# Optimization experiments

Measured on AMD Instinct MI355X. Metric: run time of the kernel, lower is better.

## Reference

```python
import jax, jax.numpy as jnp
import numpy as np

B, N, DIM, H, DH = 4, 4096, 1024, 16, 64
INNER = H * DH


def setup_inputs() -> dict:
    key = jax.random.key(0)
    k1, k2, k3, k4 = jax.random.split(key, 4)
    x = jax.random.normal(k1, (B, N, DIM), dtype=jnp.float32)
    mask = jax.random.randint(k2, (B, N), 0, 2).astype(bool)
    Wqkv = jax.random.normal(k3, (DIM, 3 * INNER), dtype=jnp.float32) * (DIM ** -0.5)
    Wout = jax.random.normal(k4, (INNER, DIM), dtype=jnp.float32) * (INNER ** -0.5)
    bout = jnp.zeros((DIM,), dtype=jnp.float32)
    return {"x": x, "mask": mask, "Wqkv": Wqkv, "Wout": Wout, "bout": bout}


def _split_heads(t):
    b, n, _ = t.shape
    return t.reshape(b, n, H, DH).transpose(0, 2, 1, 3)  # b h n d


def reference(x, mask, Wqkv, Wout, bout):
    qkv = x @ Wqkv                      # [b, n, 3*inner]
    q, k, v = jnp.split(qkv, 3, axis=-1)
    q, k, v = map(_split_heads, (q, k, v))  # [b, h, n, d]
    q = jax.nn.elu(q) + 1.0
    k = jax.nn.elu(k) + 1.0
    m = mask[:, None, :, None]          # [b, 1, n, 1]
    k = jnp.where(m, k, 0.0)
    v = jnp.where(m, v, 0.0)
    kv = jnp.einsum('bhnd,bhne->bhde', k, v)      # [b, h, d, d]
    out = jnp.einsum('bhnd,bhde->bhne', q, kv)    # [b, h, n, d]
    z = 1.0 / (jnp.einsum('bhnd,bhd->bhn', q, k.sum(axis=2)) + 1e-6)
    out = out * z[..., None]
    out = out.transpose(0, 2, 1, 3).reshape(x.shape[0], -1, INNER)  # [b, n, inner]
    return out @ Wout + bout
```

## Files before the change

### kernel.cpp

```cpp
#include <hip/hip_runtime.h>
#include <hip/hip_bf16.h>
#include <cstddef>
#include <cstdint>

#define B_     4
#define N_     4096
#define DIM_   1024
#define H_     16
#define DH_    64
#define INNER_ 1024
#define MTOK   (B_ * N_)
#define QKVC   (3 * INNER_)
#define NCH    16
#define CHUNK  (N_ / NCH)

typedef __attribute__((ext_vector_type(8))) short short8;
typedef __attribute__((ext_vector_type(4))) float f32x4;

__device__ __forceinline__ float elu1(float x) {
    return x > 0.f ? x + 1.f : __expf(x);
}
__device__ __forceinline__ unsigned short f2bf(float f) {
    __hip_bfloat16 h = __float2bfloat16(f);
    return __builtin_bit_cast(unsigned short, h);
}
__device__ __forceinline__ float bf2f(unsigned short u) {
    __hip_bfloat16 h = __builtin_bit_cast(__hip_bfloat16, u);
    return __bfloat162float(h);
}

__device__ __forceinline__ void gload16(const void* g, void* l) {
    __builtin_amdgcn_global_load_lds(
        (const __attribute__((address_space(1))) unsigned int*)g,
        (__attribute__((address_space(3))) unsigned int*)l, 16, 0, 0);
}

__global__ __launch_bounds__(256) void cast_bf16(
    const float* __restrict__ src, unsigned short* __restrict__ dst, long n8)
{
    const long stride = (long)gridDim.x * 256;
    for (long i = (long)blockIdx.x * 256 + threadIdx.x; i < n8; i += stride) {
        const float4 f0 = reinterpret_cast<const float4*>(src)[2 * i];
        const float4 f1 = reinterpret_cast<const float4*>(src)[2 * i + 1];
        short8 u;
        u[0] = (short)f2bf(f0.x); u[1] = (short)f2bf(f0.y);
        u[2] = (short)f2bf(f0.z); u[3] = (short)f2bf(f0.w);
        u[4] = (short)f2bf(f1.x); u[5] = (short)f2bf(f1.y);
        u[6] = (short)f2bf(f1.z); u[7] = (short)f2bf(f1.w);
        reinterpret_cast<short8*>(dst)[i] = u;
    }
}

__global__ __launch_bounds__(256) void transpose_cast(
    const float* __restrict__ src, unsigned short* __restrict__ dst,
    int R, int C)
{
    __shared__ float t[32][33];
    const int r0 = blockIdx.x * 32, c0 = blockIdx.y * 32;
    const int tx = threadIdx.x & 31, ty = threadIdx.x >> 5;
#pragma unroll
    for (int i = 0; i < 4; ++i)
        t[ty * 4 + i][tx] = src[(size_t)(r0 + ty * 4 + i) * C + c0 + tx];
    __syncthreads();
#pragma unroll
    for (int i = 0; i < 4; ++i)
        dst[(size_t)(c0 + ty * 4 + i) * R + r0 + tx] = f2bf(t[tx][ty * 4 + i]);
}

template<int EPI, int HAS_BIAS>
__global__ __launch_bounds__(512, 2) void gemm256(
    const unsigned short* __restrict__ A,
    const unsigned short* __restrict__ BT,
    void* __restrict__ Cv,
    const float* __restrict__ bias,
    const int* __restrict__ msk,
    int M, int N, int K, int lda, int ldb, int ldc)
{
    __shared__ __align__(16) unsigned short smem[4][256 * 64];

    const int tid = threadIdx.x;
    const int wv  = tid >> 6;
    const int ln  = tid & 63;
    const int wr  = wv >> 2;
    const int wc  = wv & 3;

    const int nwg = gridDim.x;
    int wg = blockIdx.x;
    {
        const int q = nwg >> 3, r = nwg & 7;
        const int xcd = wg & 7, lid = wg >> 3;
        wg = (xcd < r ? xcd * (q + 1) : r * (q + 1) + (xcd - r) * q) + lid;
    }
    const int ncol = N >> 8;
    const int bx = wg % ncol;
    const int by = wg / ncol;
    const int row0 = by << 8;
    const int col0 = bx << 8;

    const int l8    = ln >> 3;
    const int sslot = ((ln & 7) ^ l8) << 3;

    const int lr16 = ln & 15;
    const int kc   = ln >> 4;
    const int sw   = lr16 & 7;
    const int soff0 = (kc ^ sw) << 3;
    const int soff1 = ((4 + kc) ^ sw) << 3;

    f32x4 acc[8][4];
#pragma unroll
    for (int m = 0; m < 8; ++m)
#pragma unroll
        for (int n = 0; n < 4; ++n) acc[m][n] = f32x4{0.f, 0.f, 0.f, 0.f};

    const int NT = K >> 6;

#pragma unroll
    for (int i = 0; i < 4; ++i) {
        const int lr = wv * 32 + i * 8;
        gload16(&A [(size_t)(row0 + lr + l8) * lda + sslot], &smem[0][lr * 64]);
        gload16(&BT[(size_t)(col0 + lr + l8) * ldb + sslot], &smem[2][lr * 64]);
    }
    __syncthreads();

    for (int t = 0; t < NT; ++t) {
        const int cur = t & 1;
        const unsigned short* bufA = smem[cur];
        const unsigned short* bufB = smem[2 + cur];
        short8 bf[4][2];
#pragma unroll
        for (int p = 0; p < 4; ++p) {
            short8 af[2][2];
#pragma unroll
            for (int mi = 0; mi < 2; ++mi) {
                const int row = wr * 128 + (p * 2 + mi) * 16 + lr16;
                af[mi][0] = *reinterpret_cast<const short8*>(&bufA[row * 64 + soff0]);
                af[mi][1] = *reinterpret_cast<const short8*>(&bufA[row * 64 + soff1]);
            }
            if (p == 0) {
#pragma unroll
                for (int n = 0; n < 4; ++n) {
                    const int row = wc * 64 + n * 16 + lr16;
                    bf[n][0] = *reinterpret_cast<const short8*>(&bufB[row * 64 + soff0]);
                    bf[n][1] = *reinterpret_cast<const short8*>(&bufB[row * 64 + soff1]);
                }
                if (t + 1 < NT) {
                    const int k0 = (t + 1) << 6;
                    unsigned short* nA = smem[cur ^ 1];
                    unsigned short* nB = smem[2 + (cur ^ 1)];
#pragma unroll
                    for (int i = 0; i < 4; ++i) {
                        const int lr = wv * 32 + i * 8;
                        gload16(&A [(size_t)(row0 + lr + l8) * lda + k0 + sslot],
                                &nA[lr * 64]);
                        gload16(&BT[(size_t)(col0 + lr + l8) * ldb + k0 + sslot],
                                &nB[lr * 64]);
                    }
                }
            }
            __builtin_amdgcn_s_barrier();
            __builtin_amdgcn_sched_barrier(0);
            __builtin_amdgcn_s_setprio(1);
#pragma unroll
            for (int mi = 0; mi < 2; ++mi)
#pragma unroll
                for (int n = 0; n < 4; ++n) {
                    acc[p * 2 + mi][n] = __builtin_amdgcn_mfma_f32_16x16x32_bf16(
                        af[mi][0], bf[n][0], acc[p * 2 + mi][n], 0, 0, 0);
                    acc[p * 2 + mi][n] = __builtin_amdgcn_mfma_f32_16x16x32_bf16(
                        af[mi][1], bf[n][1], acc[p * 2 + mi][n], 0, 0, 0);
                }
            __builtin_amdgcn_s_setprio(0);
            __builtin_amdgcn_sched_barrier(0);
            if (p < 3) {
                __builtin_amdgcn_s_barrier();
                __builtin_amdgcn_sched_barrier(0);
            }
        }
        __syncthreads();
    }

    const int orow = (ln >> 4) << 2;
    const int ocol = ln & 15;

    if constexpr (EPI == 2) {
        unsigned short* tb = &smem[0][0];
#pragma unroll
        for (int m = 0; m < 8; ++m) {
            const int rrb = wr * 128 + m * 16 + orow;
            const int4 m4 = *reinterpret_cast<const int4*>(&msk[row0 + rrb]);
            int mv[4] = { m4.x, m4.y, m4.z, m4.w };
            const int slot16 = rrb >> 3, half = (rrb >> 2) & 1;
#pragma unroll
            for (int n = 0; n < 4; ++n) {
                const int chl = wc * 64 + n * 16 + ocol;
                const bool isk = (col0 + chl) < 1024;
                ushort4 st;
#pragma unroll
                for (int r2 = 0; r2 < 4; ++r2) {
                    float o = acc[m][n][r2];
                    o = mv[r2] ? (isk ? elu1(o) : o) : 0.f;
                    ((unsigned short*)&st)[r2] = f2bf(o);
                }
                *reinterpret_cast<ushort4*>(
                    &tb[chl * 256 + ((slot16 ^ (chl & 7)) << 3) + half * 4]) = st;
            }
        }
        __syncthreads();
        unsigned short* dst = (unsigned short*)Cv;
#pragma unroll
        for (int i = 0; i < 16; ++i) {
            const int idx = i * 512 + tid;
            const int ch = idx >> 5;
            const int sl = idx & 31;
            const short8 v = *reinterpret_cast<const short8*>(
                &tb[ch * 256 + ((sl ^ (ch & 7)) << 3)]);
            *reinterpret_cast<short8*>(
                &dst[(size_t)(col0 + ch) * ldc + row0 + sl * 8]) = v;
        }
    } else {
#pragma unroll
        for (int m = 0; m < 8; ++m) {
            const int rrb = row0 + wr * 128 + m * 16 + orow;
#pragma unroll
            for (int n = 0; n < 4; ++n) {
                const int c = col0 + wc * 64 + n * 16 + ocol;
                float bv = 0.f;
                if constexpr (HAS_BIAS) bv = bias[c];
#pragma unroll
                for (int r2 = 0; r2 < 4; ++r2) {
                    const int rr = rrb + r2;
                    float o = acc[m][n][r2] + bv;
                    if constexpr (EPI == 1) {
                        o = elu1(o);
                        ((unsigned short*)Cv)[(size_t)rr * ldc + c] = f2bf(o);
                    } else {
                        ((float*)Cv)[(size_t)rr * ldc + c] = o;
                    }
                }
            }
        }
    }
}

__global__ __launch_bounds__(256) void kv_partial(
    const unsigned short* __restrict__ kvT, float* __restrict__ part)
{
    const int bh = blockIdx.x;
    const int ch = blockIdx.y;
    const int b = bh / H_, h = bh % H_;
    const int tok0 = b * N_ + ch * CHUNK;

    __shared__ __align__(16) unsigned short kt[64 * 64];
    __shared__ __align__(16) unsigned short vt[64 * 64];
    __shared__ float ksr[4][64];

    const int tid = threadIdx.x;
    const int wv = tid >> 6, ln = tid & 63;
    const int wr = wv >> 1, wc = wv & 1;
    const int l8 = ln >> 3;
    const int sslot = ((ln & 7) ^ l8) << 3;
    const int lr16 = ln & 15;
    const int kc = ln >> 4;
    const int sw = lr16 & 7;

    const size_t krow = (size_t)(h * 64) * MTOK;
    const size_t vrow = (size_t)(1024 + h * 64) * MTOK;

    f32x4 acc[2][2];
#pragma unroll
    for (int i = 0; i < 2; ++i)
#pragma unroll
        for (int j = 0; j < 2; ++j) acc[i][j] = f32x4{0.f, 0.f, 0.f, 0.f};

    const int kd = tid & 63, kq = tid >> 6;
    float ksacc = 0.f;

    for (int st = 0; st < 4; ++st) {
        const int tb = tok0 + st * 64;
        __syncthreads();
#pragma unroll
        for (int i = 0; i < 2; ++i) {
            const int rb = (wv * 2 + i) * 8;
            gload16(&kvT[krow + (size_t)(rb + l8) * MTOK + tb + sslot], &kt[rb * 64]);
            gload16(&kvT[vrow + (size_t)(rb + l8) * MTOK + tb + sslot], &vt[rb * 64]);
        }
        __syncthreads();
#pragma unroll
        for (int ks = 0; ks < 2; ++ks) {
            const int soff = ((ks * 4 + kc) ^ sw) << 3;
            short8 af[2], bf[2];
#pragma unroll
            for (int mi = 0; mi < 2; ++mi)
                af[mi] = *reinterpret_cast<const short8*>(
                    &kt[(wr * 32 + mi * 16 + lr16) * 64 + soff]);
#pragma unroll
            for (int ni = 0; ni < 2; ++ni)
                bf[ni] = *reinterpret_cast<const short8*>(
                    &vt[(wc * 32 + ni * 16 + lr16) * 64 + soff]);
#pragma unroll
            for (int mi = 0; mi < 2; ++mi)
#pragma unroll
                for (int ni = 0; ni < 2; ++ni)
                    acc[mi][ni] = __builtin_amdgcn_mfma_f32_16x16x32_bf16(
                        af[mi], bf[ni], acc[mi][ni], 0, 0, 0);
        }
#pragma unroll
        for (int sl = 0; sl < 2; ++sl) {
            const int phys = (kq * 2 + sl) ^ (kd & 7);
            short8 v = *reinterpret_cast<const short8*>(&kt[kd * 64 + phys * 8]);
#pragma unroll
            for (int e = 0; e < 8; ++e) ksacc += bf2f((unsigned short)v[e]);
        }
    }
    ksr[kq][kd] = ksacc;
    __syncthreads();

    float* p = part + ((size_t)bh * NCH + ch) * 4160;
    const int orow = (ln >> 4) << 2;
    const int ocol = ln & 15;
#pragma unroll
    for (int mi = 0; mi < 2; ++mi)
#pragma unroll
        for (int ni = 0; ni < 2; ++ni) {
            const int d0 = wr * 32 + mi * 16 + orow;
            const int e  = wc * 32 + ni * 16 + ocol;
#pragma unroll
            for (int r = 0; r < 4; ++r)
                p[(d0 + r) * 64 + e] = acc[mi][ni][r];
        }
    if (tid < 64)
        p[4096 + tid] = ksr[0][tid] + ksr[1][tid] + ksr[2][tid] + ksr[3][tid];
}

__global__ __launch_bounds__(256) void kv_reduce(
    const float* __restrict__ part, unsigned short* __restrict__ kvtb,
    float* __restrict__ ksumf)
{
    const int bh = blockIdx.x;
    for (int idx = threadIdx.x; idx < 4096; idx += 256) {
        float s = 0.f;
        for (int c = 0; c < NCH; ++c)
            s += part[((size_t)bh * NCH + c) * 4160 + idx];
        const int d = idx >> 6, e = idx & 63;
        const unsigned short hi = f2bf(s);
        const float lo = s - bf2f(hi);
        kvtb[(size_t)bh * 8192 + e * 64 + d] = hi;
        kvtb[(size_t)bh * 8192 + 4096 + e * 64 + d] = f2bf(lo);
    }
    if (threadIdx.x < 64) {
        float s = 0.f;
        for (int c = 0; c < NCH; ++c)
            s += part[((size_t)bh * NCH + c) * 4160 + 4096 + threadIdx.x];
        ksumf[bh * 64 + threadIdx.x] = s;
    }
}

__global__ __launch_bounds__(256) void attn_mfma(
    const unsigned short* __restrict__ qbf,
    const unsigned short* __restrict__ kvtb,
    const float* __restrict__ ksumf,
    unsigned short* __restrict__ attnbf)
{
    const int bh = blockIdx.x, tt = blockIdx.y;
    const int b = bh / H_, h = bh % H_;
    const int tok0 = b * N_ + tt * 256;

    __shared__ __align__(16) unsigned short qt[256 * 64];
    __shared__ float den[256];

    const int tid = threadIdx.x;
    const int wv = tid >> 6, ln = tid & 63;
    const int l8 = ln >> 3;
    const int sslot = ((ln & 7) ^ l8) << 3;
    const int lr16 = ln & 15;
    const int kc = ln >> 4;

    const unsigned short* kvb = kvtb + (size_t)bh * 8192;
    short8 bhf[4][2], blf[4][2];
#pragma unroll
    for (int n = 0; n < 4; ++n)
#pragma unroll
        for (int ks = 0; ks < 2; ++ks) {
            const int off = (n * 16 + lr16) * 64 + ks * 32 + kc * 8;
            bhf[n][ks] = *reinterpret_cast<const short8*>(&kvb[off]);
            blf[n][ks] = *reinterpret_cast<const short8*>(&kvb[4096 + off]);
        }

#pragma unroll
    for (int i = 0; i < 8; ++i) {
        const int rb = wv * 64 + i * 8;
        gload16(&qbf[(size_t)(tok0 + rb + l8) * INNER_ + h * 64 + sslot],
                &qt[rb * 64]);
    }

    {
        float dsum = 0.f;
        const unsigned short* qr = &qbf[(size_t)(tok0 + tid) * INNER_ + h * 64];
        const float* ksp = &ksumf[bh * 64];
#pragma unroll
        for (int j = 0; j < 8; ++j) {
            short8 v = *reinterpret_cast<const short8*>(&qr[j * 8]);
#pragma unroll
            for (int e = 0; e < 8; ++e)
                dsum += bf2f((unsigned short)v[e]) * ksp[j * 8 + e];
        }
        den[tid] = dsum;
    }
    __syncthreads();

    f32x4 acc[4][4];
#pragma unroll
    for (int m = 0; m < 4; ++m)
#pragma unroll
        for (int n = 0; n < 4; ++n) acc[m][n] = f32x4{0.f, 0.f, 0.f, 0.f};

#pragma unroll
    for (int ks = 0; ks < 2; ++ks) {
        const int soff = ((ks * 4 + kc) ^ (lr16 & 7)) << 3;
        short8 af[4];
#pragma unroll
        for (int m = 0; m < 4; ++m)
            af[m] = *reinterpret_cast<const short8*>(
                &qt[(wv * 64 + m * 16 + lr16) * 64 + soff]);
#pragma unroll
        for (int m = 0; m < 4; ++m)
#pragma unroll
            for (int n = 0; n < 4; ++n) {
                acc[m][n] = __builtin_amdgcn_mfma_f32_16x16x32_bf16(
                    af[m], bhf[n][ks], acc[m][n], 0, 0, 0);
                acc[m][n] = __builtin_amdgcn_mfma_f32_16x16x32_bf16(
                    af[m], blf[n][ks], acc[m][n], 0, 0, 0);
            }
    }

    const int orow = (ln >> 4) << 2;
    const int ocol = ln & 15;
#pragma unroll
    for (int m = 0; m < 4; ++m) {
        const int rl = wv * 64 + m * 16 + orow;
#pragma unroll
        for (int r = 0; r < 4; ++r) {
            const float z = 1.f / (den[rl + r] + 1e-6f);
            const size_t orow_g = (size_t)(tok0 + rl + r) * INNER_ + h * 64;
#pragma unroll
            for (int n = 0; n < 4; ++n)
                attnbf[orow_g + n * 16 + ocol] = f2bf(acc[m][n][r] * z);
        }
    }
}

extern "C" void kernel_launch(void* const* d_in, const int* in_sizes, int n_in,
                              void* d_out, int out_size, void* d_ws, size_t ws_size,
                              hipStream_t stream)
{
    const float* x    = (const float*)d_in[0];
    const int*   mask = (const int*)d_in[1];
    const float* Wqkv = (const float*)d_in[2];
    const float* Wout = (const float*)d_in[3];
    const float* bout = (const float*)d_in[4];
    float* out = (float*)d_out;

    const size_t need = 127156224;
    if (ws_size < need) return;

    char* base = (char*)d_ws;
    unsigned short* xbf    = (unsigned short*)base;
    unsigned short* attnbf = xbf;
    unsigned short* kvT    = (unsigned short*)(base + 33554432);
    unsigned short* wqkvT  = (unsigned short*)(base + 100663296);
    unsigned short* woutT  = (unsigned short*)(base + 106954752);
    float* part  = (float*)(base + 109051904);
    unsigned short* kvtb = (unsigned short*)(base + 126091264);
    float* ksumf = (float*)(base + 127139840);
    unsigned short* qbf = (unsigned short*)d_out;

    cast_bf16<<<dim3(2048), dim3(256), 0, stream>>>(
        x, xbf, (long)MTOK * DIM_ / 8);
    transpose_cast<<<dim3(32, 96), dim3(256), 0, stream>>>(Wqkv, wqkvT, DIM_, QKVC);
    transpose_cast<<<dim3(32, 32), dim3(256), 0, stream>>>(Wout, woutT, INNER_, INNER_);

    gemm256<1, 0><<<dim3(64 * 4), dim3(512), 0, stream>>>(
        xbf, wqkvT, qbf, nullptr, nullptr, MTOK, 1024, DIM_, DIM_, DIM_, 1024);
    gemm256<2, 0><<<dim3(64 * 8), dim3(512), 0, stream>>>(
        xbf, wqkvT + (size_t)1024 * 1024, kvT, nullptr, mask,
        MTOK, 2048, DIM_, DIM_, DIM_, MTOK);

    kv_partial<<<dim3(B_ * H_, NCH), dim3(256), 0, stream>>>(kvT, part);
    kv_reduce<<<dim3(B_ * H_), dim3(256), 0, stream>>>(part, kvtb, ksumf);

    attn_mfma<<<dim3(B_ * H_, N_ / 256), dim3(256), 0, stream>>>(
        qbf, kvtb, ksumf, attnbf);

    gemm256<0, 1><<<dim3(64 * 4), dim3(512), 0, stream>>>(
        attnbf, woutT, out, bout, nullptr, MTOK, INNER_, INNER_, INNER_, INNER_, INNER_);
}
```

Before: 244.0 us.

## Fuse QKV GEMMs into one launch and split K-tiles into halves with vmcnt pipelining

Merges the separate Q and KV projection GEMMs into a single 768-block launch whose epilogue branches on column block: it writes elu+1 Q row-major, or masked and transposed K/V into the kvT buffer. The GEMM main loop now stores each 64-wide K tile as two 32-wide halves with a new XOR swizzle. It prefetches per half and uses partial vmcnt waits instead of full syncthreads, aiming to overlap global loads with MFMA and cut barrier stalls. The risk is that finer-grained waits and a new swizzle could add LDS bank conflicts or sync errors, and the fused grid has mixed epilogue costs.

Result: slower. 258.7 us (+6.0%).

```diff
diff --git a/kernel.cpp b/kernel.cpp
--- a/kernel.cpp
+++ b/kernel.cpp
@@ -72,11 +72,12 @@
     const unsigned short* __restrict__ A,
     const unsigned short* __restrict__ BT,
     void* __restrict__ Cv,
+    unsigned short* __restrict__ Ckv,
     const float* __restrict__ bias,
     const int* __restrict__ msk,
     int M, int N, int K, int lda, int ldb, int ldc)
 {
-    __shared__ __align__(16) unsigned short smem[4][256 * 64];
+    __shared__ __align__(16) unsigned short smem[4][2][256 * 32];
 
     const int tid = threadIdx.x;
     const int wv  = tid >> 6;
@@ -97,14 +98,12 @@
     const int row0 = by << 8;
     const int col0 = bx << 8;
 
-    const int l8    = ln >> 3;
-    const int sslot = ((ln & 7) ^ l8) << 3;
+    const int lrow  = ln >> 2;
+    const int gslot = (((ln & 3) ^ ((ln >> 2) & 3) ^ ((ln >> 4) & 3)) << 3);
 
     const int lr16 = ln & 15;
     const int kc   = ln >> 4;
-    const int sw   = lr16 & 7;
-    const int soff0 = (kc ^ sw) << 3;
-    const int soff1 = ((4 + kc) ^ sw) << 3;
+    const int physoff = ((kc ^ ((lr16 ^ (lr16 >> 2)) & 3)) << 3);
 
     f32x4 acc[8][4];
 #pragma unroll
@@ -115,107 +114,118 @@
     const int NT = K >> 6;
 
 #pragma unroll
-    for (int i = 0; i < 4; ++i) {
-        const int lr = wv * 32 + i * 8;
-        gload16(&A [(size_t)(row0 + lr + l8) * lda + sslot], &smem[0][lr * 64]);
-        gload16(&BT[(size_t)(col0 + lr + l8) * ldb + sslot], &smem[2][lr * 64]);
-    }
-    __syncthreads();
+    for (int kh = 0; kh < 2; ++kh)
+#pragma unroll
+        for (int i = 0; i < 2; ++i) {
+            const int rowb = wv * 32 + i * 16;
+            gload16(&A [(size_t)(row0 + rowb + lrow) * lda + kh * 32 + gslot],
+                    &smem[0][kh][rowb * 32]);
+            gload16(&BT[(size_t)(col0 + rowb + lrow) * ldb + kh * 32 + gslot],
+                    &smem[2][kh][rowb * 32]);
+        }
+    asm volatile("s_waitcnt vmcnt(4)" ::: "memory");
+    __builtin_amdgcn_s_barrier();
+    __builtin_amdgcn_sched_barrier(0);
 
     for (int t = 0; t < NT; ++t) {
-        const int cur = t & 1;
-        const unsigned short* bufA = smem[cur];
-        const unsigned short* bufB = smem[2 + cur];
-        short8 bf[4][2];
-#pragma unroll
-        for (int p = 0; p < 4; ++p) {
-            short8 af[2][2];
-#pragma unroll
-            for (int mi = 0; mi < 2; ++mi) {
-                const int row = wr * 128 + (p * 2 + mi) * 16 + lr16;
-                af[mi][0] = *reinterpret_cast<const short8*>(&bufA[row * 64 + soff0]);
-                af[mi][1] = *reinterpret_cast<const short8*>(&bufA[row * 64 + soff1]);
-            }
-            if (p == 0) {
-#pragma unroll
-                for (int n = 0; n < 4; ++n) {
-                    const int row = wc * 64 + n * 16 + lr16;
-                    bf[n][0] = *reinterpret_cast<const short8*>(&bufB[row * 64 + soff0]);
-                    bf[n][1] = *reinterpret_cast<const short8*>(&bufB[row * 64 + soff1]);
+        const int buf = t & 1;
+#pragma unroll
+        for (int kh = 0; kh < 2; ++kh) {
+            const unsigned short* pA = &smem[buf][kh][0];
+            const unsigned short* pB = &smem[2 + buf][kh][0];
+            short8 af[8], bfr[4];
+#pragma unroll
+            for (int m = 0; m < 8; ++m)
+                af[m] = *reinterpret_cast<const short8*>(
+                    &pA[(wr * 128 + m * 16 + lr16) * 32 + physoff]);
+#pragma unroll
+            for (int n = 0; n < 4; ++n)
+                bfr[n] = *reinterpret_cast<const short8*>(
+                    &pB[(wc * 64 + n * 16 + lr16) * 32 + physoff]);
+            if (t + 1 < NT) {
+                const int k0 = (t + 1) * 64 + kh * 32;
+                unsigned short* nA = &smem[buf ^ 1][kh][0];
+                unsigned short* nB = &smem[2 + (buf ^ 1)][kh][0];
+#pragma unroll
+                for (int i = 0; i < 2; ++i) {
+                    const int rowb = wv * 32 + i * 16;
+                    gload16(&A [(size_t)(row0 + rowb + lrow) * lda + k0 + gslot],
+                            &nA[rowb * 32]);
+                    gload16(&BT[(size_t)(col0 + rowb + lrow) * ldb + k0 + gslot],
+                            &nB[rowb * 32]);
                 }
-                if (t + 1 < NT) {
-                    const int k0 = (t + 1) << 6;
-                    unsigned short* nA = smem[cur ^ 1];
-                    unsigned short* nB = smem[2 + (cur ^ 1)];
-#pragma unroll
-                    for (int i = 0; i < 4; ++i) {
-                        const int lr = wv * 32 + i * 8;
-                        gload16(&A [(size_t)(row0 + lr + l8) * lda + k0 + sslot],
-                                &nA[lr * 64]);
-                        gload16(&BT[(size_t)(col0 + lr + l8) * ldb + k0 + sslot],
-                                &nB[lr * 64]);
-                    }
-                }
-            }
+            }
+            __builtin_amdgcn_sched_barrier(0);
             __builtin_amdgcn_s_barrier();
             __builtin_amdgcn_sched_barrier(0);
             __builtin_amdgcn_s_setprio(1);
 #pragma unroll
-            for (int mi = 0; mi < 2; ++mi)
-#pragma unroll
-                for (int n = 0; n < 4; ++n) {
-                    acc[p * 2 + mi][n] = __builtin_amdgcn_mfma_f32_16x16x32_bf16(
-                        af[mi][0], bf[n][0], acc[p * 2 + mi][n], 0, 0, 0);
-                    acc[p * 2 + mi][n] = __builtin_amdgcn_mfma_f32_16x16x32_bf16(
-                        af[mi][1], bf[n][1], acc[p * 2 + mi][n], 0, 0, 0);
-                }
+            for (int m = 0; m < 8; ++m)
+#pragma unroll
+                for (int n = 0; n < 4; ++n)
+                    acc[m][n] = __builtin_amdgcn_mfma_f32_16x16x32_bf16(
+                        af[m], bfr[n], acc[m][n], 0, 0, 0);
             __builtin_amdgcn_s_setprio(0);
             __builtin_amdgcn_sched_barrier(0);
-            if (p < 3) {
-                __builtin_amdgcn_s_barrier();
-                __builtin_amdgcn_sched_barrier(0);
-            }
-        }
-        __syncthreads();
+            if (t + 1 < NT) asm volatile("s_waitcnt vmcnt(4)" ::: "memory");
+            else            asm volatile("s_waitcnt vmcnt(0)" ::: "memory");
+            __builtin_amdgcn_s_barrier();
+            __builtin_amdgcn_sched_barrier(0);
+        }
     }
 
     const int orow = (ln >> 4) << 2;
     const int ocol = ln & 15;
 
-    if constexpr (EPI == 2) {
-        unsigned short* tb = &smem[0][0];
-#pragma unroll
-        for (int m = 0; m < 8; ++m) {
-            const int rrb = wr * 128 + m * 16 + orow;
-            const int4 m4 = *reinterpret_cast<const int4*>(&msk[row0 + rrb]);
-            int mv[4] = { m4.x, m4.y, m4.z, m4.w };
-            const int slot16 = rrb >> 3, half = (rrb >> 2) & 1;
-#pragma unroll
-            for (int n = 0; n < 4; ++n) {
-                const int chl = wc * 64 + n * 16 + ocol;
-                const bool isk = (col0 + chl) < 1024;
-                ushort4 st;
-#pragma unroll
-                for (int r2 = 0; r2 < 4; ++r2) {
-                    float o = acc[m][n][r2];
-                    o = mv[r2] ? (isk ? elu1(o) : o) : 0.f;
-                    ((unsigned short*)&st)[r2] = f2bf(o);
+    if constexpr (EPI == 3) {
+        if (col0 < 1024) {
+            unsigned short* dst = (unsigned short*)Cv;
+#pragma unroll
+            for (int m = 0; m < 8; ++m) {
+                const int rrb = row0 + wr * 128 + m * 16 + orow;
+#pragma unroll
+                for (int n = 0; n < 4; ++n) {
+                    const int c = col0 + wc * 64 + n * 16 + ocol;
+#pragma unroll
+                    for (int r2 = 0; r2 < 4; ++r2)
+                        dst[(size_t)(rrb + r2) * ldc + c] =
+                            f2bf(elu1(acc[m][n][r2]));
                 }
-                *reinterpret_cast<ushort4*>(
-                    &tb[chl * 256 + ((slot16 ^ (chl & 7)) << 3) + half * 4]) = st;
-            }
-        }
-        __syncthreads();
-        unsigned short* dst = (unsigned short*)Cv;
-#pragma unroll
-        for (int i = 0; i < 16; ++i) {
-            const int idx = i * 512 + tid;
-            const int ch = idx >> 5;
-            const int sl = idx & 31;
-            const short8 v = *reinterpret_cast<const short8*>(
-                &tb[ch * 256 + ((sl ^ (ch & 7)) << 3)]);
-            *reinterpret_cast<short8*>(
-                &dst[(size_t)(col0 + ch) * ldc + row0 + sl * 8]) = v;
+            }
+        } else {
+            unsigned short* tb = &smem[0][0][0];
+#pragma unroll
+            for (int m = 0; m < 8; ++m) {
+                const int rrb = wr * 128 + m * 16 + orow;
+                const int4 m4 = *reinterpret_cast<const int4*>(&msk[row0 + rrb]);
+                int mv[4] = { m4.x, m4.y, m4.z, m4.w };
+                const int slot16 = rrb >> 3, half = (rrb >> 2) & 1;
+#pragma unroll
+                for (int n = 0; n < 4; ++n) {
+                    const int chl = wc * 64 + n * 16 + ocol;
+                    const bool isk = (col0 + chl) < 2048;
+                    ushort4 st;
+#pragma unroll
+                    for (int r2 = 0; r2 < 4; ++r2) {
+                        float o = acc[m][n][r2];
+                        o = mv[r2] ? (isk ? elu1(o) : o) : 0.f;
+                        ((unsigned short*)&st)[r2] = f2bf(o);
+                    }
+                    *reinterpret_cast<ushort4*>(
+                        &tb[chl * 256 + ((slot16 ^ (chl & 7)) << 3) + half * 4]) = st;
+                }
+            }
+            __syncthreads();
+#pragma unroll
+            for (int i = 0; i < 16; ++i) {
+                const int idx = i * 512 + tid;
+                const int ch = idx >> 5;
+                const int sl = idx & 31;
+                const short8 v = *reinterpret_cast<const short8*>(
+                    &tb[ch * 256 + ((sl ^ (ch & 7)) << 3)]);
+                *reinterpret_cast<short8*>(
+                    &Ckv[(size_t)(col0 - 1024 + ch) * MTOK + row0 + sl * 8]) = v;
+            }
         }
     } else {
 #pragma unroll
@@ -227,16 +237,9 @@
                 float bv = 0.f;
                 if constexpr (HAS_BIAS) bv = bias[c];
 #pragma unroll
-                for (int r2 = 0; r2 < 4; ++r2) {
-                    const int rr = rrb + r2;
-                    float o = acc[m][n][r2] + bv;
-                    if constexpr (EPI == 1) {
-                        o = elu1(o);
-                        ((unsigned short*)Cv)[(size_t)rr * ldc + c] = f2bf(o);
-                    } else {
-                        ((float*)Cv)[(size_t)rr * ldc + c] = o;
-                    }
-                }
+                for (int r2 = 0; r2 < 4; ++r2)
+                    ((float*)Cv)[(size_t)(rrb + r2) * ldc + c] =
+                        acc[m][n][r2] + bv;
             }
         }
     }
@@ -479,11 +482,9 @@
     transpose_cast<<<dim3(32, 96), dim3(256), 0, stream>>>(Wqkv, wqkvT, DIM_, QKVC);
     transpose_cast<<<dim3(32, 32), dim3(256), 0, stream>>>(Wout, woutT, INNER_, INNER_);
 
-    gemm256<1, 0><<<dim3(64 * 4), dim3(512), 0, stream>>>(
-        xbf, wqkvT, qbf, nullptr, nullptr, MTOK, 1024, DIM_, DIM_, DIM_, 1024);
-    gemm256<2, 0><<<dim3(64 * 8), dim3(512), 0, stream>>>(
-        xbf, wqkvT + (size_t)1024 * 1024, kvT, nullptr, mask,
-        MTOK, 2048, DIM_, DIM_, DIM_, MTOK);
+    gemm256<3, 0><<<dim3(64 * 12), dim3(512), 0, stream>>>(
+        xbf, wqkvT, qbf, kvT, nullptr, mask,
+        MTOK, QKVC, DIM_, DIM_, DIM_, 1024);
 
     kv_partial<<<dim3(B_ * H_, NCH), dim3(256), 0, stream>>>(kvT, part);
     kv_reduce<<<dim3(B_ * H_), dim3(256), 0, stream>>>(part, kvtb, ksumf);
@@ -492,5 +493,6 @@
         qbf, kvtb, ksumf, attnbf);
 
     gemm256<0, 1><<<dim3(64 * 4), dim3(512), 0, stream>>>(
-        attnbf, woutT, out, bout, nullptr, MTOK, INNER_, INNER_, INNER_, INNER_, INNER_);
-}
+        attnbf, woutT, out, nullptr, bout, nullptr,
+        MTOK, INNER_, INNER_, INNER_, INNER_, INNER_);
+}
```

## Fuse prep kernels and double-buffer A fragments in GEMM main loop

Applied to the files above, without the earlier changes.

Merges the x cast and the two weight transpose-casts into one launch, with branching on block index, to cut launch overhead and let the parts run concurrently. In the GEMM, the B fragments and the first A fragments are loaded and the next-tile prefetch is issued before the p loop. Within the loop, the A fragments for step p+1 are loaded while the MFMAs for step p run, and several sched_barriers and s_barriers are dropped. This aims to hide LDS latency behind MFMA work, at the cost of more registers and less explicit control over instruction scheduling.

New measurement: 237.7 us. 1.03x faster.

```diff
diff --git a/kernel.cpp b/kernel.cpp
--- a/kernel.cpp
+++ b/kernel.cpp
@@ -35,28 +35,38 @@
         (__attribute__((address_space(3))) unsigned int*)l, 16, 0, 0);
 }
 
-__global__ __launch_bounds__(256) void cast_bf16(
-    const float* __restrict__ src, unsigned short* __restrict__ dst, long n8)
-{
-    const long stride = (long)gridDim.x * 256;
-    for (long i = (long)blockIdx.x * 256 + threadIdx.x; i < n8; i += stride) {
-        const float4 f0 = reinterpret_cast<const float4*>(src)[2 * i];
-        const float4 f1 = reinterpret_cast<const float4*>(src)[2 * i + 1];
-        short8 u;
-        u[0] = (short)f2bf(f0.x); u[1] = (short)f2bf(f0.y);
-        u[2] = (short)f2bf(f0.z); u[3] = (short)f2bf(f0.w);
-        u[4] = (short)f2bf(f1.x); u[5] = (short)f2bf(f1.y);
-        u[6] = (short)f2bf(f1.z); u[7] = (short)f2bf(f1.w);
-        reinterpret_cast<short8*>(dst)[i] = u;
-    }
-}
-
-__global__ __launch_bounds__(256) void transpose_cast(
-    const float* __restrict__ src, unsigned short* __restrict__ dst,
-    int R, int C)
+__global__ __launch_bounds__(256) void prep_fused(
+    const float* __restrict__ x, unsigned short* __restrict__ xbf,
+    const float* __restrict__ Wqkv, unsigned short* __restrict__ wqkvT,
+    const float* __restrict__ Wout, unsigned short* __restrict__ woutT)
 {
     __shared__ float t[32][33];
-    const int r0 = blockIdx.x * 32, c0 = blockIdx.y * 32;
+    const int blk = blockIdx.x;
+    if (blk < 2048) {
+        const long n8 = (long)MTOK * DIM_ / 8;
+        const long stride = 2048L * 256;
+        for (long i = (long)blk * 256 + threadIdx.x; i < n8; i += stride) {
+            const float4 f0 = reinterpret_cast<const float4*>(x)[2 * i];
+            const float4 f1 = reinterpret_cast<const float4*>(x)[2 * i + 1];
+            short8 u;
+            u[0] = (short)f2bf(f0.x); u[1] = (short)f2bf(f0.y);
+            u[2] = (short)f2bf(f0.z); u[3] = (short)f2bf(f0.w);
+            u[4] = (short)f2bf(f1.x); u[5] = (short)f2bf(f1.y);
+            u[6] = (short)f2bf(f1.z); u[7] = (short)f2bf(f1.w);
+            reinterpret_cast<short8*>(xbf)[i] = u;
+        }
+        return;
+    }
+    const float* src; unsigned short* dst; int R, C, r0, c0;
+    if (blk < 5120) {
+        const int id = blk - 2048;
+        src = Wqkv; dst = wqkvT; R = DIM_; C = QKVC;
+        r0 = (id & 31) * 32; c0 = (id >> 5) * 32;
+    } else {
+        const int id = blk - 5120;
+        src = Wout; dst = woutT; R = INNER_; C = INNER_;
+        r0 = (id & 31) * 32; c0 = (id >> 5) * 32;
+    }
     const int tx = threadIdx.x & 31, ty = threadIdx.x >> 5;
 #pragma unroll
     for (int i = 0; i < 4; ++i)
@@ -127,54 +137,58 @@
         const unsigned short* bufA = smem[cur];
         const unsigned short* bufB = smem[2 + cur];
         short8 bf[4][2];
+        short8 af[2][2][2];
+
+#pragma unroll
+        for (int n = 0; n < 4; ++n) {
+            const int row = wc * 64 + n * 16 + lr16;
+            bf[n][0] = *reinterpret_cast<const short8*>(&bufB[row * 64 + soff0]);
+            bf[n][1] = *reinterpret_cast<const short8*>(&bufB[row * 64 + soff1]);
+        }
+#pragma unroll
+        for (int mi = 0; mi < 2; ++mi) {
+            const int row = wr * 128 + mi * 16 + lr16;
+            af[0][mi][0] = *reinterpret_cast<const short8*>(&bufA[row * 64 + soff0]);
+            af[0][mi][1] = *reinterpret_cast<const short8*>(&bufA[row * 64 + soff1]);
+        }
+        if (t + 1 < NT) {
+            const int k0 = (t + 1) << 6;
+            unsigned short* nA = smem[cur ^ 1];
+            unsigned short* nB = smem[2 + (cur ^ 1)];
+#pragma unroll
+            for (int i = 0; i < 4; ++i) {
+                const int lr = wv * 32 + i * 8;
+                gload16(&A [(size_t)(row0 + lr + l8) * lda + k0 + sslot],
+                        &nA[lr * 64]);
+                gload16(&BT[(size_t)(col0 + lr + l8) * ldb + k0 + sslot],
+                        &nB[lr * 64]);
+            }
+        }
+
 #pragma unroll
         for (int p = 0; p < 4; ++p) {
-            short8 af[2][2];
-#pragma unroll
-            for (int mi = 0; mi < 2; ++mi) {
-                const int row = wr * 128 + (p * 2 + mi) * 16 + lr16;
-                af[mi][0] = *reinterpret_cast<const short8*>(&bufA[row * 64 + soff0]);
-                af[mi][1] = *reinterpret_cast<const short8*>(&bufA[row * 64 + soff1]);
-            }
-            if (p == 0) {
-#pragma unroll
-                for (int n = 0; n < 4; ++n) {
-                    const int row = wc * 64 + n * 16 + lr16;
-                    bf[n][0] = *reinterpret_cast<const short8*>(&bufB[row * 64 + soff0]);
-                    bf[n][1] = *reinterpret_cast<const short8*>(&bufB[row * 64 + soff1]);
-                }
-                if (t + 1 < NT) {
-                    const int k0 = (t + 1) << 6;
-                    unsigned short* nA = smem[cur ^ 1];
-                    unsigned short* nB = smem[2 + (cur ^ 1)];
-#pragma unroll
-                    for (int i = 0; i < 4; ++i) {
-                        const int lr = wv * 32 + i * 8;
-                        gload16(&A [(size_t)(row0 + lr + l8) * lda + k0 + sslot],
-                                &nA[lr * 64]);
-                        gload16(&BT[(size_t)(col0 + lr + l8) * ldb + k0 + sslot],
-                                &nB[lr * 64]);
-                    }
+            if (p > 0) __builtin_amdgcn_s_barrier();
+            if (p < 3) {
+#pragma unroll
+                for (int mi = 0; mi < 2; ++mi) {
+                    const int row = wr * 128 + ((p + 1) * 2 + mi) * 16 + lr16;
+                    af[(p + 1) & 1][mi][0] =
+                        *reinterpret_cast<const short8*>(&bufA[row * 64 + soff0]);
+                    af[(p + 1) & 1][mi][1] =
+                        *reinterpret_cast<const short8*>(&bufA[row * 64 + soff1]);
                 }
             }
-            __builtin_amdgcn_s_barrier();
-            __builtin_amdgcn_sched_barrier(0);
             __builtin_amdgcn_s_setprio(1);
 #pragma unroll
             for (int mi = 0; mi < 2; ++mi)
 #pragma unroll
                 for (int n = 0; n < 4; ++n) {
                     acc[p * 2 + mi][n] = __builtin_amdgcn_mfma_f32_16x16x32_bf16(
-                        af[mi][0], bf[n][0], acc[p * 2 + mi][n], 0, 0, 0);
+                        af[p & 1][mi][0], bf[n][0], acc[p * 2 + mi][n], 0, 0, 0);
                     acc[p * 2 + mi][n] = __builtin_amdgcn_mfma_f32_16x16x32_bf16(
-                        af[mi][1], bf[n][1], acc[p * 2 + mi][n], 0, 0, 0);
+                        af[p & 1][mi][1], bf[n][1], acc[p * 2 + mi][n], 0, 0, 0);
                 }
             __builtin_amdgcn_s_setprio(0);
-            __builtin_amdgcn_sched_barrier(0);
-            if (p < 3) {
-                __builtin_amdgcn_s_barrier();
-                __builtin_amdgcn_sched_barrier(0);
-            }
         }
         __syncthreads();
     }
@@ -474,10 +488,8 @@
     float* ksumf = (float*)(base + 127139840);
     unsigned short* qbf = (unsigned short*)d_out;
 
-    cast_bf16<<<dim3(2048), dim3(256), 0, stream>>>(
-        x, xbf, (long)MTOK * DIM_ / 8);
-    transpose_cast<<<dim3(32, 96), dim3(256), 0, stream>>>(Wqkv, wqkvT, DIM_, QKVC);
-    transpose_cast<<<dim3(32, 32), dim3(256), 0, stream>>>(Wout, woutT, INNER_, INNER_);
+    prep_fused<<<dim3(6144), dim3(256), 0, stream>>>(
+        x, xbf, Wqkv, wqkvT, Wout, woutT);
 
     gemm256<1, 0><<<dim3(64 * 4), dim3(512), 0, stream>>>(
         xbf, wqkvT, qbf, nullptr, nullptr, MTOK, 1024, DIM_, DIM_, DIM_, 1024);
@@ -492,5 +504,6 @@
         qbf, kvtb, ksumf, attnbf);
 
     gemm256<0, 1><<<dim3(64 * 4), dim3(512), 0, stream>>>(
-        attnbf, woutT, out, bout, nullptr, MTOK, INNER_, INNER_, INNER_, INNER_, INNER_);
-}
+        attnbf, woutT, out, bout, nullptr,
+        MTOK, INNER_, INNER_, INNER_, INNER_, INNER_);
+}
```
